# Optimization experiments

Measured on AMD Instinct MI355X. Metric: run time of the kernel, lower is better.

## Reference

```python
import jax, jax.numpy as jnp
import numpy as np

B, T, D = 2, 2048, 1024
H, KVH = 16, 4
HD = D // H            # 64
E, TOPK, FFH = 8, 2, 2048
EPS = 1e-6
ROPE_THETA = 10000.0


def rmsnorm(x, w):
    return x * jax.lax.rsqrt(jnp.mean(x * x, axis=-1, keepdims=True) + EPS) * w


def rope(x, cos, sin):
    # x: (B, h, T, hd); pairs (even, odd) treated as complex, matching view_as_complex
    x2 = x.reshape(*x.shape[:-1], -1, 2)
    x0, x1 = x2[..., 0], x2[..., 1]
    o0 = x0 * cos - x1 * sin
    o1 = x0 * sin + x1 * cos
    return jnp.stack([o0, o1], axis=-1).reshape(x.shape)


def setup_inputs() -> dict:
    key = jax.random.key(0)
    ks = jax.random.split(key, 12)
    s = 0.02
    return {
        'x': jax.random.normal(ks[0], (B, T, D), dtype=jnp.float32),
        'attn_norm_w': jnp.ones((D,), jnp.float32),
        'wq': jax.random.normal(ks[1], (D, H * HD), jnp.float32) * s,
        'wk': jax.random.normal(ks[2], (D, KVH * HD), jnp.float32) * s,
        'wv': jax.random.normal(ks[3], (D, KVH * HD), jnp.float32) * s,
        'wo': jax.random.normal(ks[4], (D, D), jnp.float32) * s,
        'ffn_norm_w': jnp.ones((D,), jnp.float32),
        'gate_w': jax.random.normal(ks[5], (D, E), jnp.float32) * s,
        'gate_bias': jnp.zeros((E,), jnp.float32),  # e_score_correction_bias (aux-loss-free)
        'expert_w1': jax.random.normal(ks[6], (E, D, FFH), jnp.float32) * s,
        'expert_w2': jax.random.normal(ks[7], (E, FFH, D), jnp.float32) * s,
        'shared_w1': jax.random.normal(ks[8], (D, FFH), jnp.float32) * s,
        'shared_w2': jax.random.normal(ks[9], (FFH, D), jnp.float32) * s,
    }


def block_forward(x, attn_norm_w, wq, wk, wv, wo, ffn_norm_w, gate_w, gate_bias,
                  expert_w1, expert_w2, shared_w1, shared_w2):
    # ---- RoPE tables (precompute_freqs_cis, scaling_factor=1.0) ----
    half = HD // 2
    inv_freq = 1.0 / (ROPE_THETA ** (jnp.arange(half, dtype=jnp.float32) / half))
    t = jnp.arange(T, dtype=jnp.float32)
    fr = t[:, None] * inv_freq          # (T, half)
    cos, sin = jnp.cos(fr), jnp.sin(fr)

    # ---- attn_norm + GQA attention ----
    h = rmsnorm(x, attn_norm_w)
    q = (h @ wq).reshape(B, T, H, HD).transpose(0, 2, 1, 3)      # (B,H,T,HD)
    k = (h @ wk).reshape(B, T, KVH, HD).transpose(0, 2, 1, 3)    # (B,KVH,T,HD)
    v = (h @ wv).reshape(B, T, KVH, HD).transpose(0, 2, 1, 3)
    q = rope(q, cos, sin)
    k = rope(k, cos, sin)
    n_rep = H // KVH
    k = jnp.repeat(k, n_rep, axis=1)    # repeat_interleave over head dim
    v = jnp.repeat(v, n_rep, axis=1)
    att = jnp.einsum('bhqd,bhkd->bhqk', q, k) * (HD ** -0.5)
    causal = jnp.tril(jnp.ones((T, T), dtype=bool))
    att = jnp.where(causal, att, jnp.finfo(att.dtype).min)
    att = jax.nn.softmax(att, axis=-1)
    attn_out = jnp.einsum('bhqk,bhkd->bhqd', att, v).transpose(0, 2, 1, 3).reshape(B, T, D) @ wo
    x1 = x + attn_out

    # ---- ffn_norm + MoE feed-forward ----
    h2 = rmsnorm(x1, ffn_norm_w).reshape(-1, D)                  # (N, D)
    N = B * T
    shared = jax.nn.silu(h2 @ shared_w1) @ shared_w2             # 1 shared expert
    scores = jax.nn.sigmoid(h2 @ gate_w) + gate_bias             # sigmoid gate + correction bias
    topk_w, topk_i = jax.lax.top_k(scores, TOPK)
    topk_w = topk_w / (topk_w.sum(-1, keepdims=True) + 1e-20)    # norm_topk_prob; routed_scale=1.0
    combine = jnp.zeros((N, E), x.dtype).at[jnp.arange(N)[:, None], topk_i].add(topk_w)
    hmid = jax.nn.silu(jnp.einsum('nd,edh->enh', h2, expert_w1)) # (E,N,FFH)
    eout = jnp.einsum('enh,ehd->end', hmid, expert_w2)           # (E,N,D)
    routed = jnp.einsum('end,ne->nd', eout, combine)
    return x1 + (shared + routed).reshape(B, T, D)


def reference(x, attn_norm_w, wq, wk, wv, wo, ffn_norm_w, gate_w, gate_bias,
              expert_w1, expert_w2, shared_w1, shared_w2):
    return block_forward(x, attn_norm_w, wq, wk, wv, wo, ffn_norm_w, gate_w, gate_bias,
                         expert_w1, expert_w2, shared_w1, shared_w2)
```

## Files before the change

### kernel.cpp

```cpp
#include <hip/hip_runtime.h>
#include <math.h>

#define NTOK 4096
#define DM 1024
#define TSEQ 2048
#define NH 16
#define NKV 4
#define HDIM 64
#define NE 8
#define NFF 2048
#define QKVN 1536

typedef float f4v __attribute__((ext_vector_type(4)));
typedef short b8v __attribute__((ext_vector_type(8)));
typedef unsigned short u16;

__device__ __forceinline__ float silu_f(float v) { return v / (1.0f + expf(-v)); }

__device__ __forceinline__ u16 f2b(float f) {
    union { float f; unsigned u; } x{f};
    unsigned r = (x.u + 0x7FFFu + ((x.u >> 16) & 1u)) >> 16;
    return (u16)r;
}
__device__ __forceinline__ u16 f2bt(float f) {
    union { float f; unsigned u; } x{f};
    return (u16)(x.u >> 16);
}
__device__ __forceinline__ float b2f(u16 b) {
    union { unsigned u; float f; } x;
    x.u = ((unsigned)b) << 16;
    return x.f;
}

__device__ __forceinline__ void gload16(const void* g, void* l) {
    typedef __attribute__((address_space(1))) const void gv;
    typedef __attribute__((address_space(3))) void lv;
    __builtin_amdgcn_global_load_lds((gv*)g, (lv*)l, 16, 0, 0);
}

template <int MODE>
__global__ __launch_bounds__(256) void rmsnorm2_k(const float* __restrict__ x,
                                                  const float* __restrict__ w,
                                                  u16* __restrict__ oh, u16* __restrict__ ol,
                                                  float* __restrict__ of) {
    int row = blockIdx.x;
    int tid = threadIdx.x;
    const float4 v = ((const float4*)(x + (size_t)row * DM))[tid];
    float ss = v.x * v.x + v.y * v.y + v.z * v.z + v.w * v.w;
    for (int off = 32; off; off >>= 1) ss += __shfl_down(ss, off);
    __shared__ float red[4];
    if ((tid & 63) == 0) red[tid >> 6] = ss;
    __syncthreads();
    float tot = red[0] + red[1] + red[2] + red[3];
    float inv = rsqrtf(tot * (1.0f / DM) + 1e-6f);
    const float4 wv = ((const float4*)w)[tid];
    float o[4];
    o[0] = v.x * inv * wv.x; o[1] = v.y * inv * wv.y;
    o[2] = v.z * inv * wv.z; o[3] = v.w * inv * wv.w;
    if (MODE == 1) {
        float4 f; f.x = o[0]; f.y = o[1]; f.z = o[2]; f.w = o[3];
        ((float4*)(of + (size_t)row * DM))[tid] = f;
        ushort4 hb;
        hb.x = f2b(o[0]); hb.y = f2b(o[1]); hb.z = f2b(o[2]); hb.w = f2b(o[3]);
        ((ushort4*)(oh + (size_t)row * DM))[tid] = hb;
    } else {
        ushort4 hb, lb;
#pragma unroll
        for (int i = 0; i < 4; ++i) {
            u16 h = f2b(o[i]);
            u16 l = f2b(o[i] - b2f(h));
            ((u16*)&hb)[i] = h;
            ((u16*)&lb)[i] = l;
        }
        ((ushort4*)(oh + (size_t)row * DM))[tid] = hb;
        ((ushort4*)(ol + (size_t)row * DM))[tid] = lb;
    }
}

__global__ __launch_bounds__(256) void ropetab_k(float* __restrict__ tab) {
    int idx = blockIdx.x * 256 + threadIdx.x;
    if (idx >= TSEQ * 32) return;
    int t = idx >> 5, j = idx & 31;
    float inv = expf(-(float)j * (0.03125f * logf(10000.0f)));
    float s, c;
    sincosf((float)t * inv, &s, &c);
    tab[t * 64 + j * 2] = c;
    tab[t * 64 + j * 2 + 1] = s;
}

__global__ __launch_bounds__(256) void rope_split_k(const float* __restrict__ qkv,
                                                    const float* __restrict__ tab,
                                                    int colbase, int cols,
                                                    u16* __restrict__ oh, u16* __restrict__ ol) {
    int idx = blockIdx.x * 256 + threadIdx.x;
    int cpr = cols >> 3;
    int row = idx / cpr;
    int cc = (idx - row * cpr) << 3;
    const float* p = qkv + (size_t)row * QKVN + colbase + cc;
    const float4 a = *(const float4*)p;
    const float4 b = *(const float4*)(p + 4);
    float vv[8] = {a.x, a.y, a.z, a.w, b.x, b.y, b.z, b.w};
    int tpos = row & (TSEQ - 1);
    const float* tb = tab + tpos * 64 + ((cc & 63) >> 1) * 2;
    float ov[8];
#pragma unroll
    for (int q = 0; q < 4; ++q) {
        float c = tb[q * 2], s = tb[q * 2 + 1];
        float x0 = vv[2 * q], x1 = vv[2 * q + 1];
        ov[2 * q] = x0 * c - x1 * s;
        ov[2 * q + 1] = x0 * s + x1 * c;
    }
    ushort4 h0, h1, l0, l1;
#pragma unroll
    for (int i = 0; i < 8; ++i) {
        u16 h = f2b(ov[i]);
        u16 l = f2b(ov[i] - b2f(h));
        if (i < 4) { ((u16*)&h0)[i] = h; ((u16*)&l0)[i] = l; }
        else       { ((u16*)&h1)[i - 4] = h; ((u16*)&l1)[i - 4] = l; }
    }
    u16* po = oh + (size_t)row * cols + cc;
    u16* pl = ol + (size_t)row * cols + cc;
    *(ushort4*)po = h0; *(ushort4*)(po + 4) = h1;
    *(ushort4*)pl = l0; *(ushort4*)(pl + 4) = l1;
}

__global__ __launch_bounds__(256) void vtrans_k(const float* __restrict__ qkv,
                                                u16* __restrict__ oh, u16* __restrict__ ol) {
    __shared__ float tl[32][33];
    int c0 = blockIdx.x << 5;
    int r0 = blockIdx.y << 5;
    int lr = threadIdx.x >> 3, lc = (threadIdx.x & 7) << 2;
    const float4 v = *(const float4*)&qkv[(size_t)(r0 + lr) * QKVN + 1280 + c0 + lc];
    tl[lr][lc] = v.x; tl[lr][lc + 1] = v.y; tl[lr][lc + 2] = v.z; tl[lr][lc + 3] = v.w;
    __syncthreads();
    int b = r0 >> 11;
    size_t obase = ((size_t)(b * 256 + c0 + lr)) * TSEQ + (r0 & 2047) + lc;
    ushort4 h4, l4;
#pragma unroll
    for (int i = 0; i < 4; ++i) {
        float f = tl[lc + i][lr];
        u16 h = f2b(f);
        u16 l = f2b(f - b2f(h));
        ((u16*)&h4)[i] = h; ((u16*)&l4)[i] = l;
    }
    *(ushort4*)&oh[obase] = h4;
    *(ushort4*)&ol[obase] = l4;
}

__global__ __launch_bounds__(256) void tcast2_k(const float* __restrict__ in,
                                                u16* __restrict__ oh, u16* __restrict__ ol,
                                                int R, int C) {
    __shared__ float tl[32][33];
    int r0 = blockIdx.y << 5, c0 = blockIdx.x << 5;
    int lr = threadIdx.x >> 3, lc = (threadIdx.x & 7) << 2;
    const float4 v = *(const float4*)&in[(size_t)(r0 + lr) * C + c0 + lc];
    tl[lr][lc] = v.x; tl[lr][lc + 1] = v.y; tl[lr][lc + 2] = v.z; tl[lr][lc + 3] = v.w;
    __syncthreads();
    ushort4 h4, l4;
#pragma unroll
    for (int i = 0; i < 4; ++i) {
        float f = tl[lc + i][lr];
        u16 h = f2b(f);
        u16 l = f2b(f - b2f(h));
        ((u16*)&h4)[i] = h; ((u16*)&l4)[i] = l;
    }
    size_t ob = (size_t)(c0 + lr) * R + r0 + lc;
    *(ushort4*)&oh[ob] = h4;
    *(ushort4*)&ol[ob] = l4;
}

__global__ __launch_bounds__(256) void tcast_k(const float* __restrict__ in,
                                               u16* __restrict__ out, int R, int C) {
    size_t boff = (size_t)blockIdx.z * R * C;
    in += boff; out += boff;
    __shared__ float tl[32][33];
    int r0 = blockIdx.y << 5, c0 = blockIdx.x << 5;
    int lr = threadIdx.x >> 3, lc = (threadIdx.x & 7) << 2;
    const float4 v = *(const float4*)&in[(size_t)(r0 + lr) * C + c0 + lc];
    tl[lr][lc] = v.x; tl[lr][lc + 1] = v.y; tl[lr][lc + 2] = v.z; tl[lr][lc + 3] = v.w;
    __syncthreads();
    ushort4 o;
    o.x = f2b(tl[lc + 0][lr]); o.y = f2b(tl[lc + 1][lr]);
    o.z = f2b(tl[lc + 2][lr]); o.w = f2b(tl[lc + 3][lr]);
    *(ushort4*)&out[(size_t)(c0 + lr) * R + r0 + lc] = o;
}

template <int EPI>
__global__ __launch_bounds__(256) void sgemm_k(const u16* __restrict__ Ah,
                                               const u16* __restrict__ Al,
                                               const u16* __restrict__ Bh,
                                               const u16* __restrict__ Bl,
                                               const float* __restrict__ Rr,
                                               float* __restrict__ C,
                                               int M, int N, int K) {
    __shared__ u16 Ash[128 * 32], Asl[128 * 32], Bsh[128 * 32], Bsl[128 * 32];
    int t = threadIdx.x;
    int l = t & 63, w = t >> 6;
    int wr = w >> 1, wc = w & 1;
    int lx = l & 15, lg = l >> 4;
    int n0 = blockIdx.x * 128, m0 = blockIdx.y * 128;
    int srow = t >> 2;
    int cs = (t & 3) ^ ((srow & 3) ^ ((t >> 4) & 3));
    const u16 *agh[2], *agl[2], *bgh[2], *bgl[2];
#pragma unroll
    for (int i = 0; i < 2; ++i) {
        size_t ao = (size_t)(m0 + i * 64 + srow) * K + cs * 8;
        size_t bo = (size_t)(n0 + i * 64 + srow) * K + cs * 8;
        agh[i] = Ah + ao; agl[i] = Al + ao;
        bgh[i] = Bh + bo; bgl[i] = Bl + bo;
    }
    f4v acc[4][4];
#pragma unroll
    for (int m = 0; m < 4; ++m)
#pragma unroll
        for (int n = 0; n < 4; ++n) acc[m][n] = (f4v)0.0f;
    int keyr = (lx & 3) ^ ((lx >> 2) & 3);
    int chb = (lg ^ keyr) << 4;
    int aoff[4], boff[4];
#pragma unroll
    for (int m = 0; m < 4; ++m) aoff[m] = ((wr * 64 + m * 16 + lx) << 6) + chb;
#pragma unroll
    for (int n = 0; n < 4; ++n) boff[n] = ((wc * 64 + n * 16 + lx) << 6) + chb;
    int wb = w * 1024;
    for (int k0 = 0; k0 < K; k0 += 32) {
        __syncthreads();
        gload16(agh[0] + k0, (char*)Ash + wb);
        gload16(agh[1] + k0, (char*)Ash + wb + 4096);
        gload16(agl[0] + k0, (char*)Asl + wb);
        gload16(agl[1] + k0, (char*)Asl + wb + 4096);
        gload16(bgh[0] + k0, (char*)Bsh + wb);
        gload16(bgh[1] + k0, (char*)Bsh + wb + 4096);
        gload16(bgl[0] + k0, (char*)Bsl + wb);
        gload16(bgl[1] + k0, (char*)Bsl + wb + 4096);
        __syncthreads();
        b8v afh[4], afl[4], bfh[4], bfl[4];
#pragma unroll
        for (int m = 0; m < 4; ++m) {
            afh[m] = *(const b8v*)((const char*)Ash + aoff[m]);
            afl[m] = *(const b8v*)((const char*)Asl + aoff[m]);
        }
#pragma unroll
        for (int n = 0; n < 4; ++n) {
            bfh[n] = *(const b8v*)((const char*)Bsh + boff[n]);
            bfl[n] = *(const b8v*)((const char*)Bsl + boff[n]);
        }
#pragma unroll
        for (int m = 0; m < 4; ++m)
#pragma unroll
            for (int n = 0; n < 4; ++n) {
                acc[m][n] = __builtin_amdgcn_mfma_f32_16x16x32_bf16(afl[m], bfh[n], acc[m][n], 0, 0, 0);
                acc[m][n] = __builtin_amdgcn_mfma_f32_16x16x32_bf16(afh[m], bfl[n], acc[m][n], 0, 0, 0);
                acc[m][n] = __builtin_amdgcn_mfma_f32_16x16x32_bf16(afh[m], bfh[n], acc[m][n], 0, 0, 0);
            }
    }
#pragma unroll
    for (int m = 0; m < 4; ++m) {
        int r0l = m0 + wr * 64 + m * 16 + ((l >> 4) << 2);
#pragma unroll
        for (int n = 0; n < 4; ++n) {
            int col = n0 + wc * 64 + n * 16 + (l & 15);
            f4v c = acc[m][n];
#pragma unroll
            for (int j = 0; j < 4; ++j) {
                size_t idx = (size_t)(r0l + j) * N + col;
                float v = c[j];
                if (EPI == 2) v += Rr[idx];
                C[idx] = v;
            }
        }
    }
}

__global__ __launch_bounds__(256) void mattn_k(const u16* __restrict__ qh, const u16* __restrict__ ql,
                                               const u16* __restrict__ kh, const u16* __restrict__ kl,
                                               const u16* __restrict__ vth, const u16* __restrict__ vtl,
                                               u16* __restrict__ aoh, u16* __restrict__ aol) {
    __shared__ short plds[4][2][16][72];
    int t = threadIdx.x, l = t & 63, w = t >> 6;
    int bh = blockIdx.y, b = bh >> 4, h = bh & 15, kvh = h >> 2;
    size_t bT = (size_t)b * TSEQ;
    int lx = l & 15, lg = l >> 4;
    int qt = 31 - blockIdx.x;
    int q0 = qt * 64;
    b8v qfh[2], qfl[2];
    {
        size_t qo = (bT + q0 + w * 16 + lx) * DM + h * 64 + lg * 8;
        qfh[0] = *(const b8v*)(qh + qo);
        qfh[1] = *(const b8v*)(qh + qo + 32);
        qfl[0] = *(const b8v*)(ql + qo);
        qfl[1] = *(const b8v*)(ql + qo + 32);
    }
    f4v acc[4];
#pragma unroll
    for (int ht = 0; ht < 4; ++ht) acc[ht] = (f4v)0.0f;
    float l_r[4] = {0.0f, 0.0f, 0.0f, 0.0f};
    int qg[4];
#pragma unroll
    for (int r = 0; r < 4; ++r) qg[r] = q0 + w * 16 + lg * 4 + r;
    int ntile = qt + 1;
    for (int kt = 0; kt < ntile; ++kt) {
        int kv0 = kt << 6;
        f4v s[4];
#pragma unroll
        for (int st = 0; st < 4; ++st) {
            size_t ko = (bT + kv0 + st * 16 + lx) * 256 + kvh * 64 + lg * 8;
            b8v kf0h = *(const b8v*)(kh + ko);
            b8v kf1h = *(const b8v*)(kh + ko + 32);
            b8v kf0l = *(const b8v*)(kl + ko);
            b8v kf1l = *(const b8v*)(kl + ko + 32);
            f4v ss = (f4v)0.0f;
            ss = __builtin_amdgcn_mfma_f32_16x16x32_bf16(qfl[0], kf0h, ss, 0, 0, 0);
            ss = __builtin_amdgcn_mfma_f32_16x16x32_bf16(qfh[0], kf0l, ss, 0, 0, 0);
            ss = __builtin_amdgcn_mfma_f32_16x16x32_bf16(qfh[0], kf0h, ss, 0, 0, 0);
            ss = __builtin_amdgcn_mfma_f32_16x16x32_bf16(qfl[1], kf1h, ss, 0, 0, 0);
            ss = __builtin_amdgcn_mfma_f32_16x16x32_bf16(qfh[1], kf1l, ss, 0, 0, 0);
            ss = __builtin_amdgcn_mfma_f32_16x16x32_bf16(qfh[1], kf1h, ss, 0, 0, 0);
            s[st] = ss;
        }
        b8v vh0[4], vh1[4], vl0[4], vl1[4];
#pragma unroll
        for (int ht = 0; ht < 4; ++ht) {
            size_t vo = ((size_t)(b * 4 + kvh) * 64 + ht * 16 + lx) * TSEQ + kv0 + lg * 8;
            vh0[ht] = *(const b8v*)(vth + vo);
            vh1[ht] = *(const b8v*)(vth + vo + 32);
            vl0[ht] = *(const b8v*)(vtl + vo);
            vl1[ht] = *(const b8v*)(vtl + vo + 32);
        }
#pragma unroll
        for (int st = 0; st < 4; ++st)
#pragma unroll
            for (int r = 0; r < 4; ++r) {
                float v = s[st][r] * 0.125f;
                float p = (kv0 + st * 16 + lx > qg[r]) ? 0.0f : __expf(fminf(v, 60.0f));
                l_r[r] += p;
                u16 ph = f2bt(p);
                u16 pl = f2bt(p - b2f(ph));
                plds[w][0][lg * 4 + r][st * 16 + lx] = (short)ph;
                plds[w][1][lg * 4 + r][st * 16 + lx] = (short)pl;
            }
        __threadfence_block();
        __builtin_amdgcn_sched_barrier(0);
        b8v pf0h = *(const b8v*)&plds[w][0][lx][lg * 8];
        b8v pf1h = *(const b8v*)&plds[w][0][lx][32 + lg * 8];
        b8v pf0l = *(const b8v*)&plds[w][1][lx][lg * 8];
        b8v pf1l = *(const b8v*)&plds[w][1][lx][32 + lg * 8];
        __builtin_amdgcn_sched_barrier(0);
#pragma unroll
        for (int ht = 0; ht < 4; ++ht) {
            acc[ht] = __builtin_amdgcn_mfma_f32_16x16x32_bf16(pf0l, vh0[ht], acc[ht], 0, 0, 0);
            acc[ht] = __builtin_amdgcn_mfma_f32_16x16x32_bf16(pf0h, vl0[ht], acc[ht], 0, 0, 0);
            acc[ht] = __builtin_amdgcn_mfma_f32_16x16x32_bf16(pf0h, vh0[ht], acc[ht], 0, 0, 0);
            acc[ht] = __builtin_amdgcn_mfma_f32_16x16x32_bf16(pf1l, vh1[ht], acc[ht], 0, 0, 0);
            acc[ht] = __builtin_amdgcn_mfma_f32_16x16x32_bf16(pf1h, vl1[ht], acc[ht], 0, 0, 0);
            acc[ht] = __builtin_amdgcn_mfma_f32_16x16x32_bf16(pf1h, vh1[ht], acc[ht], 0, 0, 0);
        }
    }
#pragma unroll
    for (int r = 0; r < 4; ++r) {
        float rs = l_r[r];
        rs += __shfl_xor(rs, 1);
        rs += __shfl_xor(rs, 2);
        rs += __shfl_xor(rs, 4);
        rs += __shfl_xor(rs, 8);
        float rinv = 1.0f / rs;
#pragma unroll
        for (int ht = 0; ht < 4; ++ht) {
            size_t idx = (bT + q0 + w * 16 + lg * 4 + r) * DM + h * 64 + ht * 16 + lx;
            float v = acc[ht][r] * rinv;
            u16 hh = f2b(v);
            aoh[idx] = hh;
            aol[idx] = f2b(v - b2f(hh));
        }
    }
}

__global__ __launch_bounds__(64) void gate_k(const float* __restrict__ h2,
                                             const float* __restrict__ gw,
                                             const float* __restrict__ gb,
                                             int* __restrict__ top2i,
                                             float* __restrict__ top2w,
                                             int* __restrict__ counts) {
    int n = blockIdx.x;
    int lane = threadIdx.x;
    float acc[8] = {};
    for (int d = lane; d < DM; d += 64) {
        float hv = h2[(size_t)n * DM + d];
        const float4 g0 = ((const float4*)&gw[d * 8])[0];
        const float4 g1 = ((const float4*)&gw[d * 8])[1];
        acc[0] = fmaf(hv, g0.x, acc[0]); acc[1] = fmaf(hv, g0.y, acc[1]);
        acc[2] = fmaf(hv, g0.z, acc[2]); acc[3] = fmaf(hv, g0.w, acc[3]);
        acc[4] = fmaf(hv, g1.x, acc[4]); acc[5] = fmaf(hv, g1.y, acc[5]);
        acc[6] = fmaf(hv, g1.z, acc[6]); acc[7] = fmaf(hv, g1.w, acc[7]);
    }
#pragma unroll
    for (int e = 0; e < 8; ++e)
        for (int off = 32; off; off >>= 1) acc[e] += __shfl_down(acc[e], off);
    if (lane == 0) {
        float s[8];
#pragma unroll
        for (int e = 0; e < 8; ++e) s[e] = 1.0f / (1.0f + expf(-acc[e])) + gb[e];
        int i0 = 0;
#pragma unroll
        for (int e = 1; e < 8; ++e) if (s[e] > s[i0]) i0 = e;
        int i1 = (i0 == 0) ? 1 : 0;
#pragma unroll
        for (int e = 0; e < 8; ++e) if (e != i0 && s[e] > s[i1]) i1 = e;
        float w0 = s[i0], w1 = s[i1];
        float norm = 1.0f / (w0 + w1 + 1e-20f);
        top2i[n * 2] = i0; top2i[n * 2 + 1] = i1;
        top2w[n * 2] = w0 * norm; top2w[n * 2 + 1] = w1 * norm;
        atomicAdd(&counts[i0], 1);
        atomicAdd(&counts[i1], 1);
    }
}

__global__ void zero16_k(int* p) { if (threadIdx.x < 16) p[threadIdx.x] = 0; }

__global__ void scan_k(const int* __restrict__ counts, int* __restrict__ segs) {
    if (threadIdx.x == 0) {
        segs[0] = 0;
        for (int e = 0; e < NE; ++e) segs[e + 1] = segs[e] + counts[e];
    }
}

__global__ void scatter_k(const int* __restrict__ top2i, const float* __restrict__ top2w,
                          const int* __restrict__ segs, int* __restrict__ cursor,
                          int* __restrict__ list, float* __restrict__ wslot,
                          int* __restrict__ slot_of) {
    int idx = blockIdx.x * blockDim.x + threadIdx.x;
    if (idx >= NTOK * 2) return;
    int e = top2i[idx];
    int pos = segs[e] + atomicAdd(&cursor[e], 1);
    list[pos] = idx >> 1;
    wslot[pos] = top2w[idx];
    slot_of[idx] = pos;
}

template <int EPI, int MOE, int GATHER>
__global__ __launch_bounds__(256) void mgemm_k(const u16* __restrict__ A,
                                               const u16* __restrict__ Bt,
                                               const float* __restrict__ R,
                                               const float* __restrict__ wslot,
                                               const int* __restrict__ list,
                                               const int* __restrict__ segs,
                                               float* __restrict__ Cf,
                                               u16* __restrict__ Cb,
                                               int M, int N, int K) {
    __shared__ u16 As[128 * 32];
    __shared__ u16 Bs[128 * 32];
    int e = MOE ? blockIdx.z : 0;
    int base = 0, cnt = M;
    if (MOE) { base = segs[e]; cnt = segs[e + 1] - base; }
    int m0 = blockIdx.y * 128;
    if (m0 >= cnt) return;
    int n0 = blockIdx.x * 128;
    const u16* Bte = Bt + (size_t)e * N * K;
    int t = threadIdx.x;
    int l = t & 63, w = t >> 6;
    int wr = w >> 1, wc = w & 1;
    int lx = l & 15, lg = l >> 4;
    int srow = t >> 2;
    int cs = (t & 3) ^ ((srow & 3) ^ ((t >> 4) & 3));
    const u16* ag[2];
    const u16* bg[2];
#pragma unroll
    for (int i = 0; i < 2; ++i) {
        int r = m0 + i * 64 + srow;
        int ar;
        if (MOE) {
            int rc = r < cnt ? r : cnt - 1;
            ar = GATHER ? list[base + rc] : base + rc;
        } else {
            ar = r;
        }
        ag[i] = A + (size_t)ar * K + cs * 8;
        bg[i] = Bte + (size_t)(n0 + i * 64 + srow) * K + cs * 8;
    }
    f4v acc[4][4];
#pragma unroll
    for (int m = 0; m < 4; ++m)
#pragma unroll
        for (int n = 0; n < 4; ++n) acc[m][n] = (f4v)0.0f;
    int keyr = (lx & 3) ^ ((lx >> 2) & 3);
    int chb = (lg ^ keyr) << 4;
    int aoff[4], boff[4];
#pragma unroll
    for (int m = 0; m < 4; ++m) aoff[m] = ((wr * 64 + m * 16 + lx) << 6) + chb;
#pragma unroll
    for (int n = 0; n < 4; ++n) boff[n] = ((wc * 64 + n * 16 + lx) << 6) + chb;
    int wb = w * 1024;
    for (int k0 = 0; k0 < K; k0 += 32) {
        __syncthreads();
        gload16(ag[0] + k0, (char*)As + wb);
        gload16(ag[1] + k0, (char*)As + wb + 4096);
        gload16(bg[0] + k0, (char*)Bs + wb);
        gload16(bg[1] + k0, (char*)Bs + wb + 4096);
        __syncthreads();
        b8v af[4], bf[4];
#pragma unroll
        for (int m = 0; m < 4; ++m) af[m] = *(const b8v*)((const char*)As + aoff[m]);
#pragma unroll
        for (int n = 0; n < 4; ++n) bf[n] = *(const b8v*)((const char*)Bs + boff[n]);
#pragma unroll
        for (int m = 0; m < 4; ++m)
#pragma unroll
            for (int n = 0; n < 4; ++n)
                acc[m][n] = __builtin_amdgcn_mfma_f32_16x16x32_bf16(af[m], bf[n], acc[m][n], 0, 0, 0);
    }
#pragma unroll
    for (int m = 0; m < 4; ++m) {
        int r0l = m0 + wr * 64 + m * 16 + ((l >> 4) << 2);
#pragma unroll
        for (int n = 0; n < 4; ++n) {
            int col = n0 + wc * 64 + n * 16 + (l & 15);
            f4v c = acc[m][n];
#pragma unroll
            for (int j = 0; j < 4; ++j) {
                int row = r0l + j;
                if (MOE && row >= cnt) continue;
                float v = c[j];
                if (EPI == 1) {
                    v = silu_f(v);
                    Cb[(size_t)(base + row) * N + col] = f2b(v);
                } else if (EPI == 2) {
                    size_t idx = (size_t)row * N + col;
                    Cf[idx] = v + R[idx];
                } else if (EPI == 3) {
                    Cf[(size_t)(base + row) * N + col] = v * wslot[base + row];
                } else {
                    Cf[(size_t)row * N + col] = v;
                }
            }
        }
    }
}

__global__ __launch_bounds__(256) void combine_k(const float* __restrict__ eout,
                                                 const int* __restrict__ slot_of,
                                                 float* __restrict__ out) {
    int idx = blockIdx.x * blockDim.x + threadIdx.x;
    int n = idx >> 8;
    int c = idx & 255;
    const float4 a = ((const float4*)(eout + (size_t)slot_of[n * 2] * DM))[c];
    const float4 b = ((const float4*)(eout + (size_t)slot_of[n * 2 + 1] * DM))[c];
    float4 o = ((float4*)out)[idx];
    o.x += a.x + b.x; o.y += a.y + b.y; o.z += a.z + b.z; o.w += a.w + b.w;
    ((float4*)out)[idx] = o;
}

extern "C" void kernel_launch(void* const* d_in, const int* in_sizes, int n_in,
                              void* d_out, int out_size, void* d_ws, size_t ws_size,
                              hipStream_t stream) {
    (void)in_sizes; (void)n_in; (void)out_size; (void)ws_size;
    const float* x   = (const float*)d_in[0];
    const float* anw = (const float*)d_in[1];
    const float* wq  = (const float*)d_in[2];
    const float* wk  = (const float*)d_in[3];
    const float* wv  = (const float*)d_in[4];
    const float* wo  = (const float*)d_in[5];
    const float* fnw = (const float*)d_in[6];
    const float* gw  = (const float*)d_in[7];
    const float* gb  = (const float*)d_in[8];
    const float* ew1 = (const float*)d_in[9];
    const float* ew2 = (const float*)d_in[10];
    const float* sw1 = (const float*)d_in[11];
    const float* sw2 = (const float*)d_in[12];
    float* out = (float*)d_out;

#define WSOFF(mb) ((char*)d_ws + (size_t)(mb) * 1048576)
    u16* qkvT_h = (u16*)WSOFF(0);
    u16* qkvT_l = (u16*)WSOFF(3);
    u16* woT_h  = (u16*)WSOFF(6);
    u16* woT_l  = (u16*)WSOFF(8);
    u16* sw1t   = (u16*)WSOFF(10);
    u16* sw2t   = (u16*)WSOFF(14);
    u16* ew1t   = (u16*)WSOFF(18);
    u16* ew2t   = (u16*)WSOFF(50);
    float* qkv  = (float*)WSOFF(82);
    float* h2f  = (float*)WSOFF(82);
    u16* h_hi   = (u16*)WSOFF(106);
    u16* h_lo   = (u16*)WSOFF(114);
    u16* ao_hi  = (u16*)WSOFF(106);
    u16* ao_lo  = (u16*)WSOFF(114);
    u16* q_hi   = (u16*)WSOFF(122);
    u16* q_lo   = (u16*)WSOFF(130);
    u16* k_hi   = (u16*)WSOFF(138);
    u16* k_lo   = (u16*)WSOFF(140);
    u16* vT_hi  = (u16*)WSOFF(142);
    u16* vT_lo  = (u16*)WSOFF(144);
    float* x1   = (float*)WSOFF(146);
    u16* h2b    = (u16*)WSOFF(162);
    u16* midb   = (u16*)WSOFF(170);
    u16* hmidb  = (u16*)WSOFF(122);
    float* eoutb = (float*)WSOFF(154);
    int* meta0  = (int*)WSOFF(186);
    int*   top2i  = meta0;
    float* top2w  = (float*)(meta0 + 8192);
    int*   counts = meta0 + 16384;
    int*   cursor = meta0 + 16392;
    int*   segs   = meta0 + 16400;
    int*   list   = meta0 + 16416;
    float* wslot  = (float*)(meta0 + 16416 + 8192);
    int*   slot_of = meta0 + 16416 + 16384;
    float* ropetab = (float*)WSOFF(190);

    ropetab_k<<<256, 256, 0, stream>>>(ropetab);
    tcast2_k<<<dim3(32, 32), 256, 0, stream>>>(wq, qkvT_h, qkvT_l, DM, 1024);
    tcast2_k<<<dim3(8, 32), 256, 0, stream>>>(wk, qkvT_h + 1024 * 1024, qkvT_l + 1024 * 1024, DM, 256);
    tcast2_k<<<dim3(8, 32), 256, 0, stream>>>(wv, qkvT_h + 1280 * 1024, qkvT_l + 1280 * 1024, DM, 256);
    tcast2_k<<<dim3(32, 32), 256, 0, stream>>>(wo, woT_h, woT_l, DM, DM);
    tcast_k<<<dim3(NFF / 32, DM / 32, 1), 256, 0, stream>>>(sw1, sw1t, DM, NFF);
    tcast_k<<<dim3(DM / 32, NFF / 32, 1), 256, 0, stream>>>(sw2, sw2t, NFF, DM);
    tcast_k<<<dim3(NFF / 32, DM / 32, NE), 256, 0, stream>>>(ew1, ew1t, DM, NFF);
    tcast_k<<<dim3(DM / 32, NFF / 32, NE), 256, 0, stream>>>(ew2, ew2t, NFF, DM);

    rmsnorm2_k<0><<<NTOK, 256, 0, stream>>>(x, anw, h_hi, h_lo, nullptr);
    sgemm_k<0><<<dim3(QKVN / 128, NTOK / 128), 256, 0, stream>>>(
        h_hi, h_lo, qkvT_h, qkvT_l, nullptr, qkv, NTOK, QKVN, DM);
    rope_split_k<<<2048, 256, 0, stream>>>(qkv, ropetab, 0, 1024, q_hi, q_lo);
    rope_split_k<<<512, 256, 0, stream>>>(qkv, ropetab, 1024, 256, k_hi, k_lo);
    vtrans_k<<<dim3(8, 128), 256, 0, stream>>>(qkv, vT_hi, vT_lo);
    mattn_k<<<dim3(32, 32), 256, 0, stream>>>(q_hi, q_lo, k_hi, k_lo, vT_hi, vT_lo, ao_hi, ao_lo);
    sgemm_k<2><<<dim3(DM / 128, NTOK / 128), 256, 0, stream>>>(
        ao_hi, ao_lo, woT_h, woT_l, x, x1, NTOK, DM, DM);
    rmsnorm2_k<1><<<NTOK, 256, 0, stream>>>(x1, fnw, h2b, nullptr, h2f);
    zero16_k<<<1, 64, 0, stream>>>(counts);
    gate_k<<<NTOK, 64, 0, stream>>>(h2f, gw, gb, top2i, top2w, counts);
    scan_k<<<1, 1, 0, stream>>>(counts, segs);
    scatter_k<<<32, 256, 0, stream>>>(top2i, top2w, segs, cursor, list, wslot, slot_of);
    mgemm_k<1, 0, 0><<<dim3(NFF / 128, NTOK / 128, 1), 256, 0, stream>>>(
        h2b, sw1t, nullptr, nullptr, nullptr, nullptr, nullptr, midb, NTOK, NFF, DM);
    mgemm_k<2, 0, 0><<<dim3(DM / 128, NTOK / 128, 1), 256, 0, stream>>>(
        midb, sw2t, x1, nullptr, nullptr, nullptr, out, nullptr, NTOK, DM, NFF);
    mgemm_k<1, 1, 1><<<dim3(NFF / 128, NTOK / 128, NE), 256, 0, stream>>>(
        h2b, ew1t, nullptr, nullptr, list, segs, nullptr, hmidb, NTOK, NFF, DM);
    mgemm_k<3, 1, 0><<<dim3(DM / 128, NTOK / 128, NE), 256, 0, stream>>>(
        hmidb, ew2t, nullptr, wslot, nullptr, segs, eoutb, nullptr, 2 * NTOK, DM, NFF);
    combine_k<<<NTOK, 256, 0, stream>>>(eoutb, slot_of, out);
#undef WSOFF
}
```

Before: 1.230 ms.

## Split causal attention KV range across two partitions and pair query tiles per block

The attention kernel now pairs a short and a long causal query tile in each block, so every block gets about the same amount of work. It also splits each tile's KV range into two halves along a new grid z dimension. Each partition writes an unnormalized fp32 accumulator and a row-sum to workspace, and a new combine kernel adds them, normalizes, and re-splits the result into bf16 hi/lo. This removes load imbalance and raises parallelism, at the cost of extra fp32 global traffic and one more kernel launch. The softmax uses no max subtraction, so the partial results can be summed directly.

```diff
diff --git a/kernel.cpp b/kernel.cpp
--- a/kernel.cpp
+++ b/kernel.cpp
@@ -274,104 +274,133 @@
 __global__ __launch_bounds__(256) void mattn_k(const u16* __restrict__ qh, const u16* __restrict__ ql,
                                                const u16* __restrict__ kh, const u16* __restrict__ kl,
                                                const u16* __restrict__ vth, const u16* __restrict__ vtl,
-                                               u16* __restrict__ aoh, u16* __restrict__ aol) {
+                                               float* __restrict__ pacc, float* __restrict__ pl) {
     __shared__ short plds[4][2][16][72];
     int t = threadIdx.x, l = t & 63, w = t >> 6;
     int bh = blockIdx.y, b = bh >> 4, h = bh & 15, kvh = h >> 2;
+    int z = blockIdx.z;
+    size_t zoff = (size_t)z * NTOK * DM;
+    int zloff = z * NTOK * 16;
     size_t bT = (size_t)b * TSEQ;
     int lx = l & 15, lg = l >> 4;
-    int qt = 31 - blockIdx.x;
-    int q0 = qt * 64;
-    b8v qfh[2], qfl[2];
-    {
-        size_t qo = (bT + q0 + w * 16 + lx) * DM + h * 64 + lg * 8;
-        qfh[0] = *(const b8v*)(qh + qo);
-        qfh[1] = *(const b8v*)(qh + qo + 32);
-        qfl[0] = *(const b8v*)(ql + qo);
-        qfl[1] = *(const b8v*)(ql + qo + 32);
-    }
-    f4v acc[4];
-#pragma unroll
-    for (int ht = 0; ht < 4; ++ht) acc[ht] = (f4v)0.0f;
-    float l_r[4] = {0.0f, 0.0f, 0.0f, 0.0f};
-    int qg[4];
-#pragma unroll
-    for (int r = 0; r < 4; ++r) qg[r] = q0 + w * 16 + lg * 4 + r;
-    int ntile = qt + 1;
-    for (int kt = 0; kt < ntile; ++kt) {
-        int kv0 = kt << 6;
-        f4v s[4];
-#pragma unroll
-        for (int st = 0; st < 4; ++st) {
-            size_t ko = (bT + kv0 + st * 16 + lx) * 256 + kvh * 64 + lg * 8;
-            b8v kf0h = *(const b8v*)(kh + ko);
-            b8v kf1h = *(const b8v*)(kh + ko + 32);
-            b8v kf0l = *(const b8v*)(kl + ko);
-            b8v kf1l = *(const b8v*)(kl + ko + 32);
-            f4v ss = (f4v)0.0f;
-            ss = __builtin_amdgcn_mfma_f32_16x16x32_bf16(qfl[0], kf0h, ss, 0, 0, 0);
-            ss = __builtin_amdgcn_mfma_f32_16x16x32_bf16(qfh[0], kf0l, ss, 0, 0, 0);
-            ss = __builtin_amdgcn_mfma_f32_16x16x32_bf16(qfh[0], kf0h, ss, 0, 0, 0);
-            ss = __builtin_amdgcn_mfma_f32_16x16x32_bf16(qfl[1], kf1h, ss, 0, 0, 0);
-            ss = __builtin_amdgcn_mfma_f32_16x16x32_bf16(qfh[1], kf1l, ss, 0, 0, 0);
-            ss = __builtin_amdgcn_mfma_f32_16x16x32_bf16(qfh[1], kf1h, ss, 0, 0, 0);
-            s[st] = ss;
-        }
-        b8v vh0[4], vh1[4], vl0[4], vl1[4];
-#pragma unroll
-        for (int ht = 0; ht < 4; ++ht) {
-            size_t vo = ((size_t)(b * 4 + kvh) * 64 + ht * 16 + lx) * TSEQ + kv0 + lg * 8;
-            vh0[ht] = *(const b8v*)(vth + vo);
-            vh1[ht] = *(const b8v*)(vth + vo + 32);
-            vl0[ht] = *(const b8v*)(vtl + vo);
-            vl1[ht] = *(const b8v*)(vtl + vo + 32);
-        }
-#pragma unroll
-        for (int st = 0; st < 4; ++st)
-#pragma unroll
-            for (int r = 0; r < 4; ++r) {
-                float v = s[st][r] * 0.125f;
-                float p = (kv0 + st * 16 + lx > qg[r]) ? 0.0f : __expf(fminf(v, 60.0f));
-                l_r[r] += p;
-                u16 ph = f2bt(p);
-                u16 pl = f2bt(p - b2f(ph));
-                plds[w][0][lg * 4 + r][st * 16 + lx] = (short)ph;
-                plds[w][1][lg * 4 + r][st * 16 + lx] = (short)pl;
+#pragma unroll
+    for (int half = 0; half < 2; ++half) {
+        int qt = half ? (31 - blockIdx.x) : blockIdx.x;
+        int q0 = qt * 64;
+        int ntile = qt + 1;
+        int klo = (ntile * z) >> 1;
+        int khi = (ntile * (z + 1)) >> 1;
+        b8v qfh[2], qfl[2];
+        {
+            size_t qo = (bT + q0 + w * 16 + lx) * DM + h * 64 + lg * 8;
+            qfh[0] = *(const b8v*)(qh + qo);
+            qfh[1] = *(const b8v*)(qh + qo + 32);
+            qfl[0] = *(const b8v*)(ql + qo);
+            qfl[1] = *(const b8v*)(ql + qo + 32);
+        }
+        f4v acc[4];
+#pragma unroll
+        for (int ht = 0; ht < 4; ++ht) acc[ht] = (f4v)0.0f;
+        float l_r[4] = {0.0f, 0.0f, 0.0f, 0.0f};
+        int qg[4];
+#pragma unroll
+        for (int r = 0; r < 4; ++r) qg[r] = q0 + w * 16 + lg * 4 + r;
+        for (int kt = klo; kt < khi; ++kt) {
+            int kv0 = kt << 6;
+            f4v s[4];
+#pragma unroll
+            for (int st = 0; st < 4; ++st) {
+                size_t ko = (bT + kv0 + st * 16 + lx) * 256 + kvh * 64 + lg * 8;
+                b8v kf0h = *(const b8v*)(kh + ko);
+                b8v kf1h = *(const b8v*)(kh + ko + 32);
+                b8v kf0l = *(const b8v*)(kl + ko);
+                b8v kf1l = *(const b8v*)(kl + ko + 32);
+                f4v ss = (f4v)0.0f;
+                ss = __builtin_amdgcn_mfma_f32_16x16x32_bf16(qfl[0], kf0h, ss, 0, 0, 0);
+                ss = __builtin_amdgcn_mfma_f32_16x16x32_bf16(qfh[0], kf0l, ss, 0, 0, 0);
+                ss = __builtin_amdgcn_mfma_f32_16x16x32_bf16(qfh[0], kf0h, ss, 0, 0, 0);
+                ss = __builtin_amdgcn_mfma_f32_16x16x32_bf16(qfl[1], kf1h, ss, 0, 0, 0);
+                ss = __builtin_amdgcn_mfma_f32_16x16x32_bf16(qfh[1], kf1l, ss, 0, 0, 0);
+                ss = __builtin_amdgcn_mfma_f32_16x16x32_bf16(qfh[1], kf1h, ss, 0, 0, 0);
+                s[st] = ss;
             }
-        __threadfence_block();
-        __builtin_amdgcn_sched_barrier(0);
-        b8v pf0h = *(const b8v*)&plds[w][0][lx][lg * 8];
-        b8v pf1h = *(const b8v*)&plds[w][0][lx][32 + lg * 8];
-        b8v pf0l = *(const b8v*)&plds[w][1][lx][lg * 8];
-        b8v pf1l = *(const b8v*)&plds[w][1][lx][32 + lg * 8];
-        __builtin_amdgcn_sched_barrier(0);
-#pragma unroll
-        for (int ht = 0; ht < 4; ++ht) {
-            acc[ht] = __builtin_amdgcn_mfma_f32_16x16x32_bf16(pf0l, vh0[ht], acc[ht], 0, 0, 0);
-            acc[ht] = __builtin_amdgcn_mfma_f32_16x16x32_bf16(pf0h, vl0[ht], acc[ht], 0, 0, 0);
-            acc[ht] = __builtin_amdgcn_mfma_f32_16x16x32_bf16(pf0h, vh0[ht], acc[ht], 0, 0, 0);
-            acc[ht] = __builtin_amdgcn_mfma_f32_16x16x32_bf16(pf1l, vh1[ht], acc[ht], 0, 0, 0);
-            acc[ht] = __builtin_amdgcn_mfma_f32_16x16x32_bf16(pf1h, vl1[ht], acc[ht], 0, 0, 0);
-            acc[ht] = __builtin_amdgcn_mfma_f32_16x16x32_bf16(pf1h, vh1[ht], acc[ht], 0, 0, 0);
-        }
-    }
-#pragma unroll
-    for (int r = 0; r < 4; ++r) {
-        float rs = l_r[r];
-        rs += __shfl_xor(rs, 1);
-        rs += __shfl_xor(rs, 2);
-        rs += __shfl_xor(rs, 4);
-        rs += __shfl_xor(rs, 8);
-        float rinv = 1.0f / rs;
-#pragma unroll
-        for (int ht = 0; ht < 4; ++ht) {
-            size_t idx = (bT + q0 + w * 16 + lg * 4 + r) * DM + h * 64 + ht * 16 + lx;
-            float v = acc[ht][r] * rinv;
-            u16 hh = f2b(v);
-            aoh[idx] = hh;
-            aol[idx] = f2b(v - b2f(hh));
-        }
-    }
+            b8v vh0[4], vh1[4], vl0[4], vl1[4];
+#pragma unroll
+            for (int ht = 0; ht < 4; ++ht) {
+                size_t vo = ((size_t)(b * 4 + kvh) * 64 + ht * 16 + lx) * TSEQ + kv0 + lg * 8;
+                vh0[ht] = *(const b8v*)(vth + vo);
+                vh1[ht] = *(const b8v*)(vth + vo + 32);
+                vl0[ht] = *(const b8v*)(vtl + vo);
+                vl1[ht] = *(const b8v*)(vtl + vo + 32);
+            }
+#pragma unroll
+            for (int st = 0; st < 4; ++st)
+#pragma unroll
+                for (int r = 0; r < 4; ++r) {
+                    float v = s[st][r] * 0.125f;
+                    float p = (kv0 + st * 16 + lx > qg[r]) ? 0.0f : __expf(fminf(v, 60.0f));
+                    l_r[r] += p;
+                    u16 ph = f2bt(p);
+                    u16 pv = f2bt(p - b2f(ph));
+                    plds[w][0][lg * 4 + r][st * 16 + lx] = (short)ph;
+                    plds[w][1][lg * 4 + r][st * 16 + lx] = (short)pv;
+                }
+            __threadfence_block();
+            __builtin_amdgcn_sched_barrier(0);
+            b8v pf0h = *(const b8v*)&plds[w][0][lx][lg * 8];
+            b8v pf1h = *(const b8v*)&plds[w][0][lx][32 + lg * 8];
+            b8v pf0l = *(const b8v*)&plds[w][1][lx][lg * 8];
+            b8v pf1l = *(const b8v*)&plds[w][1][lx][32 + lg * 8];
+            __builtin_amdgcn_sched_barrier(0);
+#pragma unroll
+            for (int ht = 0; ht < 4; ++ht) {
+                acc[ht] = __builtin_amdgcn_mfma_f32_16x16x32_bf16(pf0l, vh0[ht], acc[ht], 0, 0, 0);
+                acc[ht] = __builtin_amdgcn_mfma_f32_16x16x32_bf16(pf0h, vl0[ht], acc[ht], 0, 0, 0);
+                acc[ht] = __builtin_amdgcn_mfma_f32_16x16x32_bf16(pf0h, vh0[ht], acc[ht], 0, 0, 0);
+                acc[ht] = __builtin_amdgcn_mfma_f32_16x16x32_bf16(pf1l, vh1[ht], acc[ht], 0, 0, 0);
+                acc[ht] = __builtin_amdgcn_mfma_f32_16x16x32_bf16(pf1h, vl1[ht], acc[ht], 0, 0, 0);
+                acc[ht] = __builtin_amdgcn_mfma_f32_16x16x32_bf16(pf1h, vh1[ht], acc[ht], 0, 0, 0);
+            }
+        }
+#pragma unroll
+        for (int r = 0; r < 4; ++r) {
+            float rs = l_r[r];
+            rs += __shfl_xor(rs, 1);
+            rs += __shfl_xor(rs, 2);
+            rs += __shfl_xor(rs, 4);
+            rs += __shfl_xor(rs, 8);
+            size_t row = bT + q0 + w * 16 + lg * 4 + r;
+            if (lx == 0) pl[zloff + row * 16 + h] = rs;
+#pragma unroll
+            for (int ht = 0; ht < 4; ++ht)
+                pacc[zoff + row * DM + h * 64 + ht * 16 + lx] = acc[ht][r];
+        }
+    }
+}
+
+__global__ __launch_bounds__(256) void atcomb_k(const float* __restrict__ pacc,
+                                                const float* __restrict__ pl,
+                                                u16* __restrict__ aoh, u16* __restrict__ aol) {
+    int row = blockIdx.x;
+    int tid = threadIdx.x;
+    int c = tid << 2;
+    int h = c >> 6;
+    float l0 = pl[row * 16 + h];
+    float l1 = pl[NTOK * 16 + row * 16 + h];
+    float rinv = 1.0f / (l0 + l1);
+    const float4 a0 = *(const float4*)&pacc[(size_t)row * DM + c];
+    const float4 a1 = *(const float4*)&pacc[(size_t)NTOK * DM + (size_t)row * DM + c];
+    float v[4] = {(a0.x + a1.x) * rinv, (a0.y + a1.y) * rinv,
+                  (a0.z + a1.z) * rinv, (a0.w + a1.w) * rinv};
+    ushort4 hb, lb;
+#pragma unroll
+    for (int i = 0; i < 4; ++i) {
+        u16 hh = f2b(v[i]);
+        ((u16*)&hb)[i] = hh;
+        ((u16*)&lb)[i] = f2b(v[i] - b2f(hh));
+    }
+    *(ushort4*)&aoh[(size_t)row * DM + c] = hb;
+    *(ushort4*)&aol[(size_t)row * DM + c] = lb;
 }
 
 __global__ __launch_bounds__(64) void gate_k(const float* __restrict__ h2,
@@ -593,6 +622,8 @@
     u16* midb   = (u16*)WSOFF(170);
     u16* hmidb  = (u16*)WSOFF(122);
     float* eoutb = (float*)WSOFF(154);
+    float* pacc = (float*)WSOFF(146);
+    float* pl   = (float*)WSOFF(178);
     int* meta0  = (int*)WSOFF(186);
     int*   top2i  = meta0;
     float* top2w  = (float*)(meta0 + 8192);
@@ -620,7 +651,8 @@
     rope_split_k<<<2048, 256, 0, stream>>>(qkv, ropetab, 0, 1024, q_hi, q_lo);
     rope_split_k<<<512, 256, 0, stream>>>(qkv, ropetab, 1024, 256, k_hi, k_lo);
     vtrans_k<<<dim3(8, 128), 256, 0, stream>>>(qkv, vT_hi, vT_lo);
-    mattn_k<<<dim3(32, 32), 256, 0, stream>>>(q_hi, q_lo, k_hi, k_lo, vT_hi, vT_lo, ao_hi, ao_lo);
+    mattn_k<<<dim3(16, 32, 2), 256, 0, stream>>>(q_hi, q_lo, k_hi, k_lo, vT_hi, vT_lo, pacc, pl);
+    atcomb_k<<<NTOK, 256, 0, stream>>>(pacc, pl, ao_hi, ao_lo);
     sgemm_k<2><<<dim3(DM / 128, NTOK / 128), 256, 0, stream>>>(
         ao_hi, ao_lo, woT_h, woT_l, x, x1, NTOK, DM, DM);
     rmsnorm2_k<1><<<NTOK, 256, 0, stream>>>(x1, fnw, h2b, nullptr, h2f);
```

Result: faster. 1.033 ms (-16.0%).
